# Performance work log

Hardware: AMD Instinct MI355X
Metric: run time of the kernel (lower is better)

Reference implementation:

```python
import jax, jax.numpy as jnp
import numpy as np

N_NODES = 50000


def sage_conv(x, src, dst, Wl, Wr, b):
    # mean-aggregate neighbor messages at destination nodes
    msg = x[src]                                            # [E, d] gather
    agg = jax.ops.segment_sum(msg, dst, num_segments=N_NODES)
    cnt = jax.ops.segment_sum(jnp.ones((src.shape[0], 1), x.dtype), dst,
                              num_segments=N_NODES)
    mean = agg / jnp.maximum(cnt, 1.0)
    # out = lin_l(mean_neighbors) + lin_r(x)
    return mean @ Wl + b + x @ Wr


def setup_inputs() -> dict:
    key = jax.random.key(0)
    ks = jax.random.split(key, 12)
    d = 64
    x = jax.random.normal(ks[0], (N_NODES, d), dtype=jnp.float32)
    edge_index = jax.random.randint(ks[1], (2, 800000), 0, N_NODES, dtype=jnp.int64)
    s = 1.0 / np.sqrt(d)
    def w(k):
        return jax.random.uniform(k, (d, d), jnp.float32, -s, s)
    return {
        "x": x, "edge_index": edge_index,
        "Wl1": w(ks[2]), "Wr1": w(ks[3]), "b1": jnp.zeros((d,), jnp.float32),
        "Wl2": w(ks[4]), "Wr2": w(ks[5]), "b2": jnp.zeros((d,), jnp.float32),
        "Wl3": w(ks[6]), "Wr3": w(ks[7]), "b3": jnp.zeros((d,), jnp.float32),
    }


def reference(x, edge_index, Wl1, Wr1, b1, Wl2, Wr2, b2, Wl3, Wr3, b3):
    src, dst = edge_index[0], edge_index[1]
    # layer 1 + ReLU (dropout in eval mode -> identity)
    h = jax.nn.relu(sage_conv(x, src, dst, Wl1, Wr1, b1))
    # layer 2 + ReLU
    h = jax.nn.relu(sage_conv(h, src, dst, Wl2, Wr2, b2))
    # final layer, no activation
    return sage_conv(h, src, dst, Wl3, Wr3, b3)
```

## Files before the change

### kernel.cpp

```cpp
#include <hip/hip_runtime.h>
#include <hip/hip_bf16.h>
#include <hip/hip_fp16.h>


#define D 64
#define NR 128
#define RSPAN 391
#define STREAM_CAP 12500
#define CAPM 96
#define SPILL_CAP 65536

typedef _Float16 half8 __attribute__((ext_vector_type(8)));
typedef float f32x4 __attribute__((ext_vector_type(4)));

__global__ __launch_bounds__(256)
void partA_kernel(const int* __restrict__ src, const int* __restrict__ dst,
                  int* __restrict__ gcur, unsigned int* __restrict__ stream_,
                  int* __restrict__ spillcnt, int2* __restrict__ spill,
                  int n_edges, int n_nodes) {
    __shared__ int hist[NR];
    __shared__ int base[NR];
    __shared__ int lcur[NR];
    const int t = threadIdx.x;
    const int e0 = blockIdx.x * 4096;

    if (t < NR) hist[t] = 0;
    __syncthreads();

#pragma unroll 4
    for (int k = 0; k < 16; k++) {
        int e = e0 + k * 256 + t;
        if (e < n_edges) {
            int d = dst[e];
            if ((unsigned)d < (unsigned)n_nodes)
                atomicAdd(&hist[d / RSPAN], 1);
        }
    }
    __syncthreads();

    if (t < NR) {
        base[t] = atomicAdd(&gcur[t], hist[t]);
        lcur[t] = 0;
    }
    __syncthreads();

#pragma unroll 4
    for (int k = 0; k < 16; k++) {
        int e = e0 + k * 256 + t;
        if (e < n_edges) {
            int d = dst[e];
            if ((unsigned)d < (unsigned)n_nodes) {
                int s = src[e];
                if ((unsigned)s >= (unsigned)n_nodes) s = 0;
                int r = d / RSPAN;
                int p = atomicAdd(&lcur[r], 1);
                int gp = base[r] + p;
                if (gp < STREAM_CAP) {
                    stream_[(size_t)r * STREAM_CAP + gp] =
                        ((unsigned)d << 16) | (unsigned)s;
                } else {
                    int q = atomicAdd(spillcnt, 1);
                    if (q < SPILL_CAP) spill[q] = make_int2(d, s);
                }
            }
        }
    }
}

__global__ __launch_bounds__(256)
void partB_kernel(const unsigned int* __restrict__ stream_,
                  const int* __restrict__ gcur,
                  const int* __restrict__ spillcnt, const int2* __restrict__ spill,
                  unsigned short* __restrict__ csrM, int* __restrict__ cntM,
                  int n_nodes) {
    __shared__ int cnt[RSPAN];
    const int t = threadIdx.x;
    const int r = blockIdx.x;
    const int n0 = r * RSPAN;

    for (int i = t; i < RSPAN; i += 256) cnt[i] = 0;
    __syncthreads();

    int total = gcur[r];
    if (total > STREAM_CAP) total = STREAM_CAP;
    const unsigned int* st = stream_ + (size_t)r * STREAM_CAP;
    for (int i = t; i < total; i += 256) {
        unsigned int e = st[i];
        int d = (int)(e >> 16);
        int p = atomicAdd(&cnt[d - n0], 1);
        if (p < CAPM) csrM[(size_t)d * CAPM + p] = (unsigned short)(e & 0xFFFF);
    }
    int sn = *spillcnt;
    if (sn > SPILL_CAP) sn = SPILL_CAP;
    for (int j = t; j < sn; j += 256) {
        int2 pr = spill[j];
        int dl = pr.x - n0;
        if ((unsigned)dl < (unsigned)RSPAN) {
            int p = atomicAdd(&cnt[dl], 1);
            if (p < CAPM) csrM[(size_t)pr.x * CAPM + p] = (unsigned short)pr.y;
        }
    }
    __syncthreads();

    for (int i = t; i < RSPAN; i += 256) {
        int n = n0 + i;
        if (n < n_nodes) cntM[n] = min(cnt[i], CAPM);
    }
}

__global__ __launch_bounds__(256)
void prep_kernel(const float* __restrict__ W0, const float* __restrict__ W1,
                 const float* __restrict__ W2, const float* __restrict__ W3,
                 const float* __restrict__ W4, const float* __restrict__ W5,
                 __half* __restrict__ WT,
                 const float* __restrict__ xin, __half* __restrict__ x16,
                 int n8) {
    if (blockIdx.x < 6) {
        const float* W;
        switch (blockIdx.x) {
            case 0: W = W0; break;
            case 1: W = W1; break;
            case 2: W = W2; break;
            case 3: W = W3; break;
            case 4: W = W4; break;
            default: W = W5; break;
        }
        __half* O = WT + blockIdx.x * D * D;
        for (int idx = threadIdx.x; idx < D * D; idx += 256) {
            int k = idx >> 6, n = idx & 63;
            O[n * D + k] = __float2half(W[idx]);
        }
        return;
    }
    int i = (blockIdx.x - 6) * blockDim.x + threadIdx.x;
    if (i >= n8) return;
    const float4* in4 = (const float4*)xin;
    float4 a = in4[2 * i];
    float4 b = in4[2 * i + 1];
    __half2 h0 = __floats2half2_rn(a.x, a.y);
    __half2 h1 = __floats2half2_rn(a.z, a.w);
    __half2 h2 = __floats2half2_rn(b.x, b.y);
    __half2 h3 = __floats2half2_rn(b.z, b.w);
    uint4 pack;
    pack.x = *(unsigned int*)&h0;
    pack.y = *(unsigned int*)&h1;
    pack.z = *(unsigned int*)&h2;
    pack.w = *(unsigned int*)&h3;
    ((uint4*)x16)[i] = pack;
}

__global__ __launch_bounds__(256)
void agg_kernel(const __half* __restrict__ h16, const int* __restrict__ cntM,
                const unsigned short* __restrict__ csrM,
                __half* __restrict__ mean16, int n_nodes) {
    int wid = (int)((blockIdx.x * (unsigned)blockDim.x + threadIdx.x) >> 6);
    int lane = threadIdx.x & 63;
    if (wid >= n_nodes) return;
    const unsigned short* nbr = csrM + (size_t)wid * CAPM;
    int cnt = cntM[wid];
    int q = lane >> 3;
    int f = lane & 7;
    const uint4* rows = (const uint4*)h16;

    float acc[8];
#pragma unroll
    for (int k = 0; k < 8; k++) acc[k] = 0.f;

    int i = q;
    for (; i + 8 < cnt; i += 16) {
        int s0 = nbr[i];
        int s1 = nbr[i + 8];
        uint4 a = rows[s0 * 8 + f];
        uint4 b = rows[s1 * 8 + f];
        const __half2* pa = (const __half2*)&a;
        const __half2* pb = (const __half2*)&b;
#pragma unroll
        for (int k = 0; k < 4; k++) {
            float2 fa = __half22float2(pa[k]);
            float2 fb = __half22float2(pb[k]);
            acc[2 * k]     += fa.x + fb.x;
            acc[2 * k + 1] += fa.y + fb.y;
        }
    }
    if (i < cnt) {
        int s0 = nbr[i];
        uint4 a = rows[s0 * 8 + f];
        const __half2* pa = (const __half2*)&a;
#pragma unroll
        for (int k = 0; k < 4; k++) {
            float2 fa = __half22float2(pa[k]);
            acc[2 * k]     += fa.x;
            acc[2 * k + 1] += fa.y;
        }
    }

#pragma unroll
    for (int m = 8; m < 64; m <<= 1) {
#pragma unroll
        for (int k = 0; k < 8; k++) acc[k] += __shfl_xor(acc[k], m, 64);
    }

    if (lane < 8) {
        float inv = 1.0f / (float)max(cnt, 1);
        __half2 p0 = __floats2half2_rn(acc[0] * inv, acc[1] * inv);
        __half2 p1 = __floats2half2_rn(acc[2] * inv, acc[3] * inv);
        __half2 p2 = __floats2half2_rn(acc[4] * inv, acc[5] * inv);
        __half2 p3 = __floats2half2_rn(acc[6] * inv, acc[7] * inv);
        uint4 pack;
        pack.x = *(unsigned int*)&p0;
        pack.y = *(unsigned int*)&p1;
        pack.z = *(unsigned int*)&p2;
        pack.w = *(unsigned int*)&p3;
        ((uint4*)mean16)[wid * 8 + lane] = pack;
    }
}

__global__ __launch_bounds__(256)
void gemm_mfma_kernel(const __half* __restrict__ mean16,
                      const __half* __restrict__ hown16,
                      const __half* __restrict__ WlT, const __half* __restrict__ WrT,
                      const float* __restrict__ bias, float* __restrict__ out32,
                      __half* __restrict__ out16, int relu, int n_nodes) {
    const int t = threadIdx.x;
    const int lane = t & 63;
    const int wave = t >> 6;
    const int quad = lane >> 4;
    const int c16  = lane & 15;
    const int row0 = blockIdx.x * 64 + wave * 16;

    int arow = row0 + c16;
    if (arow >= n_nodes) arow = n_nodes - 1;

    const half8* M  = (const half8*)mean16;
    const half8* H  = (const half8*)hown16;
    const half8* BL = (const half8*)WlT;
    const half8* BR = (const half8*)WrT;

    half8 am0 = M[arow * 8 + quad];
    half8 am1 = M[arow * 8 + 4 + quad];
    half8 ah0 = H[arow * 8 + quad];
    half8 ah1 = H[arow * 8 + 4 + quad];

    f32x4 acc[4];
#pragma unroll
    for (int nt = 0; nt < 4; nt++) {
        int col = nt * 16 + c16;
        half8 bl0 = BL[col * 8 + quad];
        half8 bl1 = BL[col * 8 + 4 + quad];
        half8 br0 = BR[col * 8 + quad];
        half8 br1 = BR[col * 8 + 4 + quad];
        f32x4 a = {0.f, 0.f, 0.f, 0.f};
        a = __builtin_amdgcn_mfma_f32_16x16x32_f16(am0, bl0, a, 0, 0, 0);
        a = __builtin_amdgcn_mfma_f32_16x16x32_f16(am1, bl1, a, 0, 0, 0);
        a = __builtin_amdgcn_mfma_f32_16x16x32_f16(ah0, br0, a, 0, 0, 0);
        a = __builtin_amdgcn_mfma_f32_16x16x32_f16(ah1, br1, a, 0, 0, 0);
        acc[nt] = a;
    }

#pragma unroll
    for (int nt = 0; nt < 4; nt++) {
        int col = nt * 16 + c16;
        float bv = bias[col];
#pragma unroll
        for (int r = 0; r < 4; r++) {
            int orow = row0 + quad * 4 + r;
            if (orow < n_nodes) {
                float v = acc[nt][r] + bv;
                if (relu) v = fmaxf(v, 0.f);
                if (out32) out32[orow * D + col] = v;
                if (out16) out16[orow * D + col] = __float2half(v);
            }
        }
    }
}

extern "C" void kernel_launch(void* const* d_in, const int* in_sizes, int n_in,
                              void* d_out, int out_size, void* d_ws, size_t ws_size,
                              hipStream_t stream) {
    const float* x  = (const float*)d_in[0];
    const int*   ei = (const int*)d_in[1];
    const int n_nodes = in_sizes[0] / D;
    const int n_edges = in_sizes[1] / 2;
    const int* src = ei;
    const int* dst = ei + n_edges;

    const float* Wl1 = (const float*)d_in[2];
    const float* Wr1 = (const float*)d_in[3];
    const float* b1  = (const float*)d_in[4];
    const float* Wl2 = (const float*)d_in[5];
    const float* Wr2 = (const float*)d_in[6];
    const float* b2  = (const float*)d_in[7];
    const float* Wl3 = (const float*)d_in[8];
    const float* Wr3 = (const float*)d_in[9];
    const float* b3  = (const float*)d_in[10];

    char* w = (char*)d_ws;
    auto alloc = [&](size_t bytes) -> char* {
        char* p = w;
        w += (bytes + 255) & ~(size_t)255;
        return p;
    };
    int*  gcur     = (int*)alloc((size_t)(NR + 1) * 4);
    int*  spillcnt = gcur + NR;
    int2* spill    = (int2*)alloc((size_t)SPILL_CAP * 8);
    unsigned int* stream_ = (unsigned int*)alloc((size_t)NR * STREAM_CAP * 4);
    int*  cntM     = (int*)alloc((size_t)n_nodes * 4);
    unsigned short* csrM = (unsigned short*)alloc((size_t)n_nodes * CAPM * 2);
    __half* x16    = (__half*)alloc((size_t)n_nodes * D * 2);
    __half* h116   = (__half*)alloc((size_t)n_nodes * D * 2);
    __half* h216   = (__half*)alloc((size_t)n_nodes * D * 2);
    __half* mean16 = (__half*)alloc((size_t)n_nodes * D * 2);
    __half* WT     = (__half*)alloc((size_t)6 * D * D * 2);

    const int pa_blocks = (n_edges + 4095) / 4096;
    const int n8  = n_nodes * D / 8;
    const int pb  = 6 + (n8 + 255) / 256;
    const int agg_blocks  = (n_nodes + 3) / 4;
    const int gemm_blocks = (n_nodes + 63) / 64;

    __half* WlT1 = WT + 0 * D * D;
    __half* WrT1 = WT + 1 * D * D;
    __half* WlT2 = WT + 2 * D * D;
    __half* WrT2 = WT + 3 * D * D;
    __half* WlT3 = WT + 4 * D * D;
    __half* WrT3 = WT + 5 * D * D;

    hipMemsetAsync(gcur, 0, (size_t)(NR + 1) * 4, stream);
    partA_kernel<<<pa_blocks, 256, 0, stream>>>(src, dst, gcur, stream_,
                                                spillcnt, spill, n_edges, n_nodes);
    partB_kernel<<<NR, 256, 0, stream>>>(stream_, gcur, spillcnt, spill,
                                         csrM, cntM, n_nodes);
    prep_kernel<<<pb, 256, 0, stream>>>(Wl1, Wr1, Wl2, Wr2, Wl3, Wr3, WT, x, x16, n8);

    agg_kernel<<<agg_blocks, 256, 0, stream>>>(x16, cntM, csrM, mean16, n_nodes);
    gemm_mfma_kernel<<<gemm_blocks, 256, 0, stream>>>(mean16, x16, WlT1, WrT1, b1,
                                                      (float*)nullptr, h116, 1, n_nodes);

    agg_kernel<<<agg_blocks, 256, 0, stream>>>(h116, cntM, csrM, mean16, n_nodes);
    gemm_mfma_kernel<<<gemm_blocks, 256, 0, stream>>>(mean16, h116, WlT2, WrT2, b2,
                                                      (float*)nullptr, h216, 1, n_nodes);

    agg_kernel<<<agg_blocks, 256, 0, stream>>>(h216, cntM, csrM, mean16, n_nodes);
    gemm_mfma_kernel<<<gemm_blocks, 256, 0, stream>>>(mean16, h216, WlT3, WrT3, b3,
                                                      (float*)d_out, (__half*)nullptr, 0, n_nodes);
}
```

Measured before the change: 226.8 us.

## Fuse neighbor aggregation and MFMA GEMM into one per-layer kernel via LDS

Result: faster. 215.2 us (-5.1%).

```diff
diff --git a/kernel.cpp b/kernel.cpp
--- a/kernel.cpp
+++ b/kernel.cpp
@@ -9,6 +9,7 @@
 #define STREAM_CAP 12500
 #define CAPM 96
 #define SPILL_CAP 65536
+#define LSTRIDE 72
 
 typedef _Float16 half8 __attribute__((ext_vector_type(8)));
 typedef float f32x4 __attribute__((ext_vector_type(4)));
@@ -112,7 +113,7 @@
 void prep_kernel(const float* __restrict__ W0, const float* __restrict__ W1,
                  const float* __restrict__ W2, const float* __restrict__ W3,
                  const float* __restrict__ W4, const float* __restrict__ W5,
-                 __half* __restrict__ WT,
+                 __half* __restrict__ WT, int* __restrict__ gcur,
                  const float* __restrict__ xin, __half* __restrict__ x16,
                  int n8) {
     if (blockIdx.x < 6) {
@@ -132,7 +133,11 @@
         }
         return;
     }
-    int i = (blockIdx.x - 6) * blockDim.x + threadIdx.x;
+    if (blockIdx.x == 6) {
+        if (threadIdx.x <= NR) gcur[threadIdx.x] = 0;
+        return;
+    }
+    int i = (blockIdx.x - 7) * blockDim.x + threadIdx.x;
     if (i >= n8) return;
     const float4* in4 = (const float4*)xin;
     float4 a = in4[2 * i];
@@ -149,127 +154,118 @@
     ((uint4*)x16)[i] = pack;
 }
 
-__global__ __launch_bounds__(256)
-void agg_kernel(const __half* __restrict__ h16, const int* __restrict__ cntM,
-                const unsigned short* __restrict__ csrM,
-                __half* __restrict__ mean16, int n_nodes) {
-    int wid = (int)((blockIdx.x * (unsigned)blockDim.x + threadIdx.x) >> 6);
-    int lane = threadIdx.x & 63;
-    if (wid >= n_nodes) return;
-    const unsigned short* nbr = csrM + (size_t)wid * CAPM;
-    int cnt = cntM[wid];
-    int q = lane >> 3;
-    int f = lane & 7;
-    const uint4* rows = (const uint4*)h16;
-
-    float acc[8];
-#pragma unroll
-    for (int k = 0; k < 8; k++) acc[k] = 0.f;
-
-    int i = q;
-    for (; i + 8 < cnt; i += 16) {
-        int s0 = nbr[i];
-        int s1 = nbr[i + 8];
-        uint4 a = rows[s0 * 8 + f];
-        uint4 b = rows[s1 * 8 + f];
-        const __half2* pa = (const __half2*)&a;
-        const __half2* pb = (const __half2*)&b;
-#pragma unroll
-        for (int k = 0; k < 4; k++) {
-            float2 fa = __half22float2(pa[k]);
-            float2 fb = __half22float2(pb[k]);
-            acc[2 * k]     += fa.x + fb.x;
-            acc[2 * k + 1] += fa.y + fb.y;
-        }
-    }
-    if (i < cnt) {
-        int s0 = nbr[i];
-        uint4 a = rows[s0 * 8 + f];
-        const __half2* pa = (const __half2*)&a;
-#pragma unroll
-        for (int k = 0; k < 4; k++) {
-            float2 fa = __half22float2(pa[k]);
-            acc[2 * k]     += fa.x;
-            acc[2 * k + 1] += fa.y;
-        }
-    }
-
-#pragma unroll
-    for (int m = 8; m < 64; m <<= 1) {
-#pragma unroll
-        for (int k = 0; k < 8; k++) acc[k] += __shfl_xor(acc[k], m, 64);
-    }
-
-    if (lane < 8) {
-        float inv = 1.0f / (float)max(cnt, 1);
-        __half2 p0 = __floats2half2_rn(acc[0] * inv, acc[1] * inv);
-        __half2 p1 = __floats2half2_rn(acc[2] * inv, acc[3] * inv);
-        __half2 p2 = __floats2half2_rn(acc[4] * inv, acc[5] * inv);
-        __half2 p3 = __floats2half2_rn(acc[6] * inv, acc[7] * inv);
-        uint4 pack;
-        pack.x = *(unsigned int*)&p0;
-        pack.y = *(unsigned int*)&p1;
-        pack.z = *(unsigned int*)&p2;
-        pack.w = *(unsigned int*)&p3;
-        ((uint4*)mean16)[wid * 8 + lane] = pack;
-    }
-}
-
-__global__ __launch_bounds__(256)
-void gemm_mfma_kernel(const __half* __restrict__ mean16,
-                      const __half* __restrict__ hown16,
-                      const __half* __restrict__ WlT, const __half* __restrict__ WrT,
-                      const float* __restrict__ bias, float* __restrict__ out32,
-                      __half* __restrict__ out16, int relu, int n_nodes) {
+__global__ __launch_bounds__(256, 6)
+void layer_kernel(const __half* __restrict__ h16, const int* __restrict__ cntM,
+                  const unsigned short* __restrict__ csrM,
+                  const __half* __restrict__ WlT, const __half* __restrict__ WrT,
+                  const float* __restrict__ bias, float* __restrict__ out32,
+                  __half* __restrict__ out16, int relu, int n_nodes) {
+    __shared__ _Float16 smean[16 * LSTRIDE];
+
     const int t = threadIdx.x;
     const int lane = t & 63;
     const int wave = t >> 6;
+    const int nb0 = blockIdx.x * 16;
+
+    const int q = lane >> 3;
+    const int f = lane & 7;
+    const uint4* rows = (const uint4*)h16;
+
+    for (int j = 0; j < 4; j++) {
+        const int row = wave * 4 + j;
+        const int node = nb0 + row;
+        float acc[8];
+#pragma unroll
+        for (int k = 0; k < 8; k++) acc[k] = 0.f;
+        int cnt = 0;
+        if (node < n_nodes) {
+            cnt = cntM[node];
+            const unsigned short* nbr = csrM + (size_t)node * CAPM;
+            int i = q;
+            for (; i + 8 < cnt; i += 16) {
+                int s0 = nbr[i];
+                int s1 = nbr[i + 8];
+                uint4 a = rows[s0 * 8 + f];
+                uint4 b = rows[s1 * 8 + f];
+                const __half2* pa = (const __half2*)&a;
+                const __half2* pb = (const __half2*)&b;
+#pragma unroll
+                for (int k = 0; k < 4; k++) {
+                    float2 fa = __half22float2(pa[k]);
+                    float2 fb = __half22float2(pb[k]);
+                    acc[2 * k]     += fa.x + fb.x;
+                    acc[2 * k + 1] += fa.y + fb.y;
+                }
+            }
+            if (i < cnt) {
+                int s0 = nbr[i];
+                uint4 a = rows[s0 * 8 + f];
+                const __half2* pa = (const __half2*)&a;
+#pragma unroll
+                for (int k = 0; k < 4; k++) {
+                    float2 fa = __half22float2(pa[k]);
+                    acc[2 * k]     += fa.x;
+                    acc[2 * k + 1] += fa.y;
+                }
+            }
+        }
+#pragma unroll
+        for (int m = 8; m < 64; m <<= 1) {
+#pragma unroll
+            for (int k = 0; k < 8; k++) acc[k] += __shfl_xor(acc[k], m, 64);
+        }
+        if (lane < 8) {
+            float inv = 1.0f / (float)max(cnt, 1);
+            __half2 p0 = __floats2half2_rn(acc[0] * inv, acc[1] * inv);
+            __half2 p1 = __floats2half2_rn(acc[2] * inv, acc[3] * inv);
+            __half2 p2 = __floats2half2_rn(acc[4] * inv, acc[5] * inv);
+            __half2 p3 = __floats2half2_rn(acc[6] * inv, acc[7] * inv);
+            uint4 pack;
+            pack.x = *(unsigned int*)&p0;
+            pack.y = *(unsigned int*)&p1;
+            pack.z = *(unsigned int*)&p2;
+            pack.w = *(unsigned int*)&p3;
+            *(uint4*)((char*)smean + row * (LSTRIDE * 2) + f * 16) = pack;
+        }
+    }
+
+    __syncthreads();
+
     const int quad = lane >> 4;
     const int c16  = lane & 15;
-    const int row0 = blockIdx.x * 64 + wave * 16;
-
-    int arow = row0 + c16;
+
+    half8 am0 = *(const half8*)((const char*)smean + c16 * (LSTRIDE * 2) + quad * 16);
+    half8 am1 = *(const half8*)((const char*)smean + c16 * (LSTRIDE * 2) + 64 + quad * 16);
+
+    int arow = nb0 + c16;
     if (arow >= n_nodes) arow = n_nodes - 1;
-
-    const half8* M  = (const half8*)mean16;
-    const half8* H  = (const half8*)hown16;
+    const half8* H = (const half8*)h16;
+    half8 ah0 = H[arow * 8 + quad];
+    half8 ah1 = H[arow * 8 + 4 + quad];
+
+    const int col = wave * 16 + c16;
     const half8* BL = (const half8*)WlT;
     const half8* BR = (const half8*)WrT;
-
-    half8 am0 = M[arow * 8 + quad];
-    half8 am1 = M[arow * 8 + 4 + quad];
-    half8 ah0 = H[arow * 8 + quad];
-    half8 ah1 = H[arow * 8 + 4 + quad];
-
-    f32x4 acc[4];
-#pragma unroll
-    for (int nt = 0; nt < 4; nt++) {
-        int col = nt * 16 + c16;
-        half8 bl0 = BL[col * 8 + quad];
-        half8 bl1 = BL[col * 8 + 4 + quad];
-        half8 br0 = BR[col * 8 + quad];
-        half8 br1 = BR[col * 8 + 4 + quad];
-        f32x4 a = {0.f, 0.f, 0.f, 0.f};
-        a = __builtin_amdgcn_mfma_f32_16x16x32_f16(am0, bl0, a, 0, 0, 0);
-        a = __builtin_amdgcn_mfma_f32_16x16x32_f16(am1, bl1, a, 0, 0, 0);
-        a = __builtin_amdgcn_mfma_f32_16x16x32_f16(ah0, br0, a, 0, 0, 0);
-        a = __builtin_amdgcn_mfma_f32_16x16x32_f16(ah1, br1, a, 0, 0, 0);
-        acc[nt] = a;
-    }
-
-#pragma unroll
-    for (int nt = 0; nt < 4; nt++) {
-        int col = nt * 16 + c16;
-        float bv = bias[col];
-#pragma unroll
-        for (int r = 0; r < 4; r++) {
-            int orow = row0 + quad * 4 + r;
-            if (orow < n_nodes) {
-                float v = acc[nt][r] + bv;
-                if (relu) v = fmaxf(v, 0.f);
-                if (out32) out32[orow * D + col] = v;
-                if (out16) out16[orow * D + col] = __float2half(v);
-            }
+    half8 bl0 = BL[col * 8 + quad];
+    half8 bl1 = BL[col * 8 + 4 + quad];
+    half8 br0 = BR[col * 8 + quad];
+    half8 br1 = BR[col * 8 + 4 + quad];
+
+    f32x4 a = {0.f, 0.f, 0.f, 0.f};
+    a = __builtin_amdgcn_mfma_f32_16x16x32_f16(am0, bl0, a, 0, 0, 0);
+    a = __builtin_amdgcn_mfma_f32_16x16x32_f16(am1, bl1, a, 0, 0, 0);
+    a = __builtin_amdgcn_mfma_f32_16x16x32_f16(ah0, br0, a, 0, 0, 0);
+    a = __builtin_amdgcn_mfma_f32_16x16x32_f16(ah1, br1, a, 0, 0, 0);
+
+    float bv = bias[col];
+#pragma unroll
+    for (int r = 0; r < 4; r++) {
+        int orow = nb0 + quad * 4 + r;
+        if (orow < n_nodes) {
+            float v = a[r] + bv;
+            if (relu) v = fmaxf(v, 0.f);
+            if (out32) out32[orow * D + col] = v;
+            if (out16) out16[orow * D + col] = __float2half(v);
         }
     }
 }
@@ -309,14 +305,12 @@
     __half* x16    = (__half*)alloc((size_t)n_nodes * D * 2);
     __half* h116   = (__half*)alloc((size_t)n_nodes * D * 2);
     __half* h216   = (__half*)alloc((size_t)n_nodes * D * 2);
-    __half* mean16 = (__half*)alloc((size_t)n_nodes * D * 2);
     __half* WT     = (__half*)alloc((size_t)6 * D * D * 2);
 
     const int pa_blocks = (n_edges + 4095) / 4096;
     const int n8  = n_nodes * D / 8;
-    const int pb  = 6 + (n8 + 255) / 256;
-    const int agg_blocks  = (n_nodes + 3) / 4;
-    const int gemm_blocks = (n_nodes + 63) / 64;
+    const int pb  = 7 + (n8 + 255) / 256;
+    const int layer_blocks = (n_nodes + 15) / 16;
 
     __half* WlT1 = WT + 0 * D * D;
     __half* WrT1 = WT + 1 * D * D;
@@ -325,22 +319,17 @@
     __half* WlT3 = WT + 4 * D * D;
     __half* WrT3 = WT + 5 * D * D;
 
-    hipMemsetAsync(gcur, 0, (size_t)(NR + 1) * 4, stream);
+    prep_kernel<<<pb, 256, 0, stream>>>(Wl1, Wr1, Wl2, Wr2, Wl3, Wr3, WT, gcur,
+                                        x, x16, n8);
     partA_kernel<<<pa_blocks, 256, 0, stream>>>(src, dst, gcur, stream_,
                                                 spillcnt, spill, n_edges, n_nodes);
     partB_kernel<<<NR, 256, 0, stream>>>(stream_, gcur, spillcnt, spill,
                                          csrM, cntM, n_nodes);
-    prep_kernel<<<pb, 256, 0, stream>>>(Wl1, Wr1, Wl2, Wr2, Wl3, Wr3, WT, x, x16, n8);
-
-    agg_kernel<<<agg_blocks, 256, 0, stream>>>(x16, cntM, csrM, mean16, n_nodes);
-    gemm_mfma_kernel<<<gemm_blocks, 256, 0, stream>>>(mean16, x16, WlT1, WrT1, b1,
-                                                      (float*)nullptr, h116, 1, n_nodes);
-
-    agg_kernel<<<agg_blocks, 256, 0, stream>>>(h116, cntM, csrM, mean16, n_nodes);
-    gemm_mfma_kernel<<<gemm_blocks, 256, 0, stream>>>(mean16, h116, WlT2, WrT2, b2,
-                                                      (float*)nullptr, h216, 1, n_nodes);
-
-    agg_kernel<<<agg_blocks, 256, 0, stream>>>(h216, cntM, csrM, mean16, n_nodes);
-    gemm_mfma_kernel<<<gemm_blocks, 256, 0, stream>>>(mean16, h216, WlT3, WrT3, b3,
-                                                      (float*)d_out, (__half*)nullptr, 0, n_nodes);
-}
+
+    layer_kernel<<<layer_blocks, 256, 0, stream>>>(x16, cntM, csrM, WlT1, WrT1, b1,
+                                                   (float*)nullptr, h116, 1, n_nodes);
+    layer_kernel<<<layer_blocks, 256, 0, stream>>>(h116, cntM, csrM, WlT2, WrT2, b2,
+                                                   (float*)nullptr, h216, 1, n_nodes);
+    layer_kernel<<<layer_blocks, 256, 0, stream>>>(h216, cntM, csrM, WlT3, WrT3, b3,
+                                                   (float*)d_out, (__half*)nullptr, 0, n_nodes);
+}
```
